# Optimization experiments

Hardware: AMD Instinct MI355X
Metric: run time of the kernel (lower is better)

## Reference

```python
import jax, jax.numpy as jnp
import numpy as np

BS, SEQ, IN, H, L = 32, 512, 1024, 1024, 2
STDV = 1.0 / np.sqrt(H)


def setup_inputs() -> dict:
    key = jax.random.key(0)
    ks = jax.random.split(key, 5)
    # params are uniform(-stdv, stdv) per reset_parameters
    u = lambda k, shape: jax.random.uniform(k, shape, jnp.float32, -STDV, STDV)
    return {
        "x": jax.random.normal(ks[0], (BS, SEQ, IN), jnp.float32),
        "w_ih": u(ks[1], (L, H, IN)),   # layer 0: [H, IN]; layer >0 uses [H, H] (IN==H here)
        "w_hh": u(ks[2], (L, H, H)),
        "b_ih": u(ks[3], (L, H)),
        "b_hh": u(ks[4], (L, H)),
    }


def _run_layer(x_sbH, w_ih_l, w_hh_l, b_ih_l, b_hh_l):
    # x_sbH: [seq, bs, in]. Precompute input projection as one GEMM.
    xproj = jnp.einsum('sbi,hi->sbh', x_sbH, w_ih_l) + b_ih_l + b_hh_l  # [seq, bs, H]

    def step(h, xp_t):
        # h_t = tanh(W_ih x_t + b_ih + W_hh h_{t-1} + b_hh)
        h_new = jnp.tanh(xp_t + h @ w_hh_l.T)
        return h_new, h_new

    h0 = jnp.zeros((x_sbH.shape[1], w_hh_l.shape[0]), x_sbH.dtype)
    h_last, hs = jax.lax.scan(step, h0, xproj)
    return hs, h_last  # hs: [seq, bs, H]


def reference(x, w_ih, w_hh, b_ih, b_hh):
    # batch_first: transpose to [seq, bs, in]
    h = jnp.transpose(x, (1, 0, 2))
    finals = []
    num_layers = w_ih.shape[0]
    for l in range(num_layers):
        h, h_last = _run_layer(h, w_ih[l], w_hh[l], b_ih[l], b_hh[l])
        finals.append(h_last)
    output = jnp.transpose(h, (1, 0, 2))           # [bs, seq, H]
    h_n = jnp.stack(finals, axis=0)                # [num_layers, bs, H]
    return output, h_n
```

## Files before the change

### kernel.cpp

```cpp
#include <hip/hip_runtime.h>

#define SEQL 512
#define BSZ  32
#define HID  1024
#define NWORK 48
#define NLAUNCH 384
#define HN_OFF 16777216

#define XPS_OFF 0u
#define H0B_OFF 33554432u
#define H1B_OFF 67108864u
#define FLG_OFF 100663296u
#define BOOT_OFF 100794368u

using f32x4  = __attribute__((ext_vector_type(4))) float;
using u16x8  = __attribute__((ext_vector_type(8))) unsigned short;
using u32x4  = __attribute__((ext_vector_type(4))) unsigned int;
using bf16x8 = __attribute__((ext_vector_type(8))) __bf16;

__device__ __forceinline__ f32x4 mfma16(u16x8 a, u16x8 b, f32x4 c) {
  return __builtin_amdgcn_mfma_f32_16x16x32_bf16(
      __builtin_bit_cast(bf16x8, a), __builtin_bit_cast(bf16x8, b), c, 0, 0, 0);
}

__device__ __forceinline__ unsigned short f2bf(float f) {
  unsigned u = __builtin_bit_cast(unsigned, f);
  u += 0x7fffu + ((u >> 16) & 1u);
  return (unsigned short)(u >> 16);
}
__device__ __forceinline__ unsigned short f2h(float f) {
  _Float16 h = (_Float16)f;
  return __builtin_bit_cast(unsigned short, h);
}
__device__ __forceinline__ float h2f(unsigned short u) {
  return (float)__builtin_bit_cast(_Float16, u);
}

__device__ __forceinline__ float tanh_fast(float x) {
  float cx = fminf(fmaxf(x, -15.f), 15.f);
  float e = __expf(2.f * cx);
  return __fdividef(e - 1.f, e + 1.f);
}

__device__ __forceinline__ void ld_tile_sc0(const unsigned short* base, u32x4 (&r)[16]) {
  const char* b0 = (const char*)base;
  const char* b1 = b0 + 16 * HID * 2;
  asm volatile(
    "global_load_dwordx4 %0, %16, off sc0\n\t"
    "global_load_dwordx4 %1, %16, off offset:64 sc0\n\t"
    "global_load_dwordx4 %2, %16, off offset:128 sc0\n\t"
    "global_load_dwordx4 %3, %16, off offset:192 sc0\n\t"
    "global_load_dwordx4 %4, %16, off offset:256 sc0\n\t"
    "global_load_dwordx4 %5, %16, off offset:320 sc0\n\t"
    "global_load_dwordx4 %6, %16, off offset:384 sc0\n\t"
    "global_load_dwordx4 %7, %16, off offset:448 sc0\n\t"
    "global_load_dwordx4 %8, %17, off sc0\n\t"
    "global_load_dwordx4 %9, %17, off offset:64 sc0\n\t"
    "global_load_dwordx4 %10, %17, off offset:128 sc0\n\t"
    "global_load_dwordx4 %11, %17, off offset:192 sc0\n\t"
    "global_load_dwordx4 %12, %17, off offset:256 sc0\n\t"
    "global_load_dwordx4 %13, %17, off offset:320 sc0\n\t"
    "global_load_dwordx4 %14, %17, off offset:384 sc0\n\t"
    "global_load_dwordx4 %15, %17, off offset:448 sc0\n\t"
    "s_waitcnt vmcnt(0)"
    : "=&v"(r[0]), "=&v"(r[1]), "=&v"(r[2]), "=&v"(r[3]),
      "=&v"(r[4]), "=&v"(r[5]), "=&v"(r[6]), "=&v"(r[7]),
      "=&v"(r[8]), "=&v"(r[9]), "=&v"(r[10]), "=&v"(r[11]),
      "=&v"(r[12]), "=&v"(r[13]), "=&v"(r[14]), "=&v"(r[15])
    : "v"(b0), "v"(b1)
    : "memory");
}

__device__ __forceinline__ u16x8 ld8h_sc0(const void* p) {
  u32x4 r;
  asm volatile("global_load_dwordx4 %0, %1, off sc0\n\ts_waitcnt vmcnt(0)"
               : "=&v"(r) : "v"(p) : "memory");
  return __builtin_bit_cast(u16x8, r);
}

__device__ __forceinline__ void flag_set(unsigned* p) {
  __hip_atomic_store(p, 1u, __ATOMIC_RELAXED, __HIP_MEMORY_SCOPE_AGENT);
}
__device__ __forceinline__ unsigned flag_get(const unsigned* p) {
  return __hip_atomic_load(p, __ATOMIC_RELAXED, __HIP_MEMORY_SCOPE_AGENT);
}

__device__ __forceinline__ void wg_wait16(const unsigned* flt, int tid) {
  if (tid < 64) {
    const unsigned* p = flt + (tid & 15);
    while (!__all(flag_get(p) != 0u)) __builtin_amdgcn_s_sleep(1);
  }
  __syncthreads();
}
__device__ __forceinline__ void wg_wait1(const unsigned* p, int tid) {
  if (tid < 64) {
    while (!__all(flag_get(p) != 0u)) __builtin_amdgcn_s_sleep(1);
  }
  __syncthreads();
}

__global__ void init_kernel(unsigned* flg, int* boot) {
  int i = blockIdx.x * 256 + threadIdx.x;
  flg[i] = 0u;
  if (blockIdx.x == 0 && threadIdx.x < 18)
    boot[threadIdx.x] = (threadIdx.x == 16) ? -1 : 0;
}

__global__ __launch_bounds__(256, 2)
void xproj_gemm(const float* __restrict__ X,
                const float* __restrict__ W,
                const float* __restrict__ bih,
                const float* __restrict__ bhh,
                unsigned short* __restrict__ out)
{
  __shared__ unsigned short sA[128 * 32];
  __shared__ unsigned short sB[128 * 32];
  const int tid  = threadIdx.x;
  const int lane = tid & 63;
  const int wave = tid >> 6;
  const int wm = wave >> 1, wn = wave & 1;
  const int bm = blockIdx.x >> 3;
  const int bn = blockIdx.x & 7;
  const int l15 = lane & 15;
  const int koff = (lane >> 4) * 8;
  const int srow = tid >> 2;
  const int skc  = (tid & 3) * 8;

  f32x4 acc[4][4];
#pragma unroll
  for (int i = 0; i < 4; ++i)
#pragma unroll
    for (int j = 0; j < 4; ++j) acc[i][j] = (f32x4)0.f;

  for (int k0 = 0; k0 < HID; k0 += 32) {
#pragma unroll
    for (int r = 0; r < 2; ++r) {
      int row = r * 64 + srow;
      int Mrow = bm * 128 + row;
      const float* src = X + ((size_t)(Mrow & 31) * SEQL + (Mrow >> 5)) * HID + k0 + skc;
      float4 a = ((const float4*)src)[0];
      float4 b = ((const float4*)src)[1];
      u16x8 av;
      av[0]=f2bf(a.x); av[1]=f2bf(a.y); av[2]=f2bf(a.z); av[3]=f2bf(a.w);
      av[4]=f2bf(b.x); av[5]=f2bf(b.y); av[6]=f2bf(b.z); av[7]=f2bf(b.w);
      *(u16x8*)&sA[row * 32 + skc] = av;

      const float* wsrc = W + (size_t)(bn * 128 + row) * HID + k0 + skc;
      float4 wa = ((const float4*)wsrc)[0];
      float4 wb = ((const float4*)wsrc)[1];
      u16x8 wv;
      wv[0]=f2bf(wa.x); wv[1]=f2bf(wa.y); wv[2]=f2bf(wa.z); wv[3]=f2bf(wa.w);
      wv[4]=f2bf(wb.x); wv[5]=f2bf(wb.y); wv[6]=f2bf(wb.z); wv[7]=f2bf(wb.w);
      *(u16x8*)&sB[row * 32 + skc] = wv;
    }
    __syncthreads();

    u16x8 af[4], bfr[4];
#pragma unroll
    for (int mt = 0; mt < 4; ++mt)
      af[mt] = *(const u16x8*)&sA[(wm * 64 + mt * 16 + l15) * 32 + koff];
#pragma unroll
    for (int nt = 0; nt < 4; ++nt)
      bfr[nt] = *(const u16x8*)&sB[(wn * 64 + nt * 16 + l15) * 32 + koff];
#pragma unroll
    for (int mt = 0; mt < 4; ++mt)
#pragma unroll
      for (int nt = 0; nt < 4; ++nt)
        acc[mt][nt] = mfma16(af[mt], bfr[nt], acc[mt][nt]);
    __syncthreads();
  }

#pragma unroll
  for (int nt = 0; nt < 4; ++nt) {
    int colg = bn * 128 + wn * 64 + nt * 16 + l15;
    float bias = bih[colg] + bhh[colg];
#pragma unroll
    for (int mt = 0; mt < 4; ++mt) {
#pragma unroll
      for (int i = 0; i < 4; ++i) {
        int rowg = bm * 128 + wm * 64 + mt * 16 + (lane >> 4) * 4 + i;
        out[(size_t)rowg * HID + colg] = f2h(acc[mt][nt][i] + bias);
      }
    }
  }
}

__global__ __launch_bounds__(256, 2)
void fused_scan(unsigned short* __restrict__ xps,
                const float* __restrict__ whh0,
                const float* __restrict__ wih1,
                const float* __restrict__ whh1,
                const float* __restrict__ bih1,
                const float* __restrict__ bhh1,
                unsigned short* __restrict__ h0b,
                unsigned short* __restrict__ h1b,
                float* __restrict__ out,
                unsigned* __restrict__ flg,
                int* __restrict__ boot)
{
  const int tid  = threadIdx.x;

  __shared__ int s_role;
  if (tid == 0) {
    unsigned xcc;
    asm volatile("s_getreg_b32 %0, hwreg(HW_REG_XCC_ID)" : "=s"(xcc));
    xcc &= 15u;
    int slot = __hip_atomic_fetch_add(&boot[(int)xcc], 1, __ATOMIC_RELAXED,
                                      __HIP_MEMORY_SCOPE_AGENT);
    if (slot == NWORK - 1) {
      int exp = -1;
      __hip_atomic_compare_exchange_strong(&boot[16], &exp, (int)xcc,
          __ATOMIC_RELAXED, __ATOMIC_RELAXED, __HIP_MEMORY_SCOPE_AGENT);
    }
    int ch;
    while ((ch = __hip_atomic_load(&boot[16], __ATOMIC_RELAXED,
                                   __HIP_MEMORY_SCOPE_AGENT)) < 0)
      __builtin_amdgcn_s_sleep(8);
    s_role = ((int)xcc == ch && slot < NWORK) ? slot : -1;
  }
  __syncthreads();
  const int role = s_role;
  if (role < 0) return;

  const int lane = tid & 63;
  const int wave = tid >> 6;
  const int l15  = lane & 15;
  const int l4   = lane >> 4;
  const int stage = role >> 4;
  const int wg    = role & 15;
  const int col0  = wg * 64;
  const int kbase = wave * 256;
  const int frow  = tid >> 3;
  const int fcb   = (tid & 7) * 8;
  const int laneoff = l15 * HID + kbase + l4 * 8;

  unsigned* flA = flg;
  unsigned* flB = flg + SEQL * 16;
  unsigned* flC = flg + 2 * SEQL * 16;

  __shared__ float red[4][32][68];

  const float* Wsl = (stage == 0) ? whh0 : (stage == 1) ? wih1 : whh1;
  u16x8 Bf[4][8];
#pragma unroll
  for (int nt = 0; nt < 4; ++nt)
#pragma unroll
    for (int ks = 0; ks < 8; ++ks) {
      const float* src = Wsl + (size_t)(col0 + nt * 16 + l15) * HID + kbase + ks * 32 + l4 * 8;
      float4 a = ((const float4*)src)[0];
      float4 b = ((const float4*)src)[1];
      u16x8 v;
      v[0]=f2bf(a.x); v[1]=f2bf(a.y); v[2]=f2bf(a.z); v[3]=f2bf(a.w);
      v[4]=f2bf(b.x); v[5]=f2bf(b.y); v[6]=f2bf(b.z); v[7]=f2bf(b.w);
      Bf[nt][ks] = v;
    }

  if (stage == 0) {
    u16x8 xh = *(const u16x8*)(xps + (size_t)frow * HID + col0 + fcb);
    for (int t = 0; t < SEQL; ++t) {
      f32x4 acc[2][4];
#pragma unroll
      for (int m = 0; m < 2; ++m)
#pragma unroll
        for (int n = 0; n < 4; ++n) acc[m][n] = (f32x4)0.f;
      if (t > 0) {
        wg_wait16(flA + (t - 1) * 16, tid);
        u32x4 r[16];
        ld_tile_sc0(h0b + (size_t)(t - 1) * (BSZ * HID) + laneoff, r);
#pragma unroll
        for (int ks = 0; ks < 8; ++ks)
#pragma unroll
          for (int m = 0; m < 2; ++m)
#pragma unroll
            for (int n = 0; n < 4; ++n)
              acc[m][n] = mfma16(__builtin_bit_cast(u16x8, r[m * 8 + ks]), Bf[n][ks], acc[m][n]);
      }
#pragma unroll
      for (int m = 0; m < 2; ++m)
#pragma unroll
        for (int n = 0; n < 4; ++n)
#pragma unroll
          for (int q = 0; q < 4; ++q)
            red[wave][m * 16 + l4 * 4 + q][n * 16 + l15] = acc[m][n][q];
      __syncthreads();
      float hv[8];
#pragma unroll
      for (int jj = 0; jj < 2; ++jj) {
        float4 r0 = *(const float4*)&red[0][frow][fcb + jj * 4];
        float4 r1 = *(const float4*)&red[1][frow][fcb + jj * 4];
        float4 r2 = *(const float4*)&red[2][frow][fcb + jj * 4];
        float4 r3 = *(const float4*)&red[3][frow][fcb + jj * 4];
        hv[jj*4+0] = r0.x + r1.x + r2.x + r3.x;
        hv[jj*4+1] = r0.y + r1.y + r2.y + r3.y;
        hv[jj*4+2] = r0.z + r1.z + r2.z + r3.z;
        hv[jj*4+3] = r0.w + r1.w + r2.w + r3.w;
      }
#pragma unroll
      for (int j = 0; j < 8; ++j) hv[j] = tanh_fast(hv[j] + h2f((unsigned short)xh[j]));
      u16x8 hb;
#pragma unroll
      for (int j = 0; j < 8; ++j) hb[j] = f2bf(hv[j]);
      *(u16x8*)(h0b + (size_t)t * (BSZ * HID) + (size_t)frow * HID + col0 + fcb) = hb;
      if (t == SEQL - 1) {
        float* o = out + HN_OFF + (size_t)frow * HID + col0 + fcb;
        ((float4*)o)[0] = make_float4(hv[0], hv[1], hv[2], hv[3]);
        ((float4*)o)[1] = make_float4(hv[4], hv[5], hv[6], hv[7]);
      } else {
        xh = *(const u16x8*)(xps + ((size_t)(t + 1) * BSZ + frow) * HID + col0 + fcb);
      }
      asm volatile("s_waitcnt vmcnt(0)" ::: "memory");
      __syncthreads();
      if (tid == 0) flag_set(&flA[t * 16 + wg]);
    }
  } else if (stage == 1) {
    float bia[8];
#pragma unroll
    for (int j = 0; j < 8; ++j)
      bia[j] = bih1[col0 + fcb + j] + bhh1[col0 + fcb + j];
    for (int t = 0; t < SEQL; ++t) {
      wg_wait16(flA + t * 16, tid);
      u32x4 r[16];
      ld_tile_sc0(h0b + (size_t)t * (BSZ * HID) + laneoff, r);
      f32x4 acc[2][4];
#pragma unroll
      for (int m = 0; m < 2; ++m)
#pragma unroll
        for (int n = 0; n < 4; ++n) acc[m][n] = (f32x4)0.f;
#pragma unroll
      for (int ks = 0; ks < 8; ++ks)
#pragma unroll
        for (int m = 0; m < 2; ++m)
#pragma unroll
          for (int n = 0; n < 4; ++n)
            acc[m][n] = mfma16(__builtin_bit_cast(u16x8, r[m * 8 + ks]), Bf[n][ks], acc[m][n]);
#pragma unroll
      for (int m = 0; m < 2; ++m)
#pragma unroll
        for (int n = 0; n < 4; ++n)
#pragma unroll
          for (int q = 0; q < 4; ++q)
            red[wave][m * 16 + l4 * 4 + q][n * 16 + l15] = acc[m][n][q];
      __syncthreads();
      float sv[8];
#pragma unroll
      for (int jj = 0; jj < 2; ++jj) {
        float4 r0 = *(const float4*)&red[0][frow][fcb + jj * 4];
        float4 r1 = *(const float4*)&red[1][frow][fcb + jj * 4];
        float4 r2 = *(const float4*)&red[2][frow][fcb + jj * 4];
        float4 r3 = *(const float4*)&red[3][frow][fcb + jj * 4];
        sv[jj*4+0] = r0.x + r1.x + r2.x + r3.x;
        sv[jj*4+1] = r0.y + r1.y + r2.y + r3.y;
        sv[jj*4+2] = r0.z + r1.z + r2.z + r3.z;
        sv[jj*4+3] = r0.w + r1.w + r2.w + r3.w;
      }
      u16x8 xo;
#pragma unroll
      for (int j = 0; j < 8; ++j) xo[j] = f2h(sv[j] + bia[j]);
      *(u16x8*)(xps + ((size_t)t * BSZ + frow) * HID + col0 + fcb) = xo;
      asm volatile("s_waitcnt vmcnt(0)" ::: "memory");
      __syncthreads();
      if (tid == 0) flag_set(&flB[t * 16 + wg]);
    }
  } else {
    for (int t = 0; t < SEQL; ++t) {
      f32x4 acc[2][4];
#pragma unroll
      for (int m = 0; m < 2; ++m)
#pragma unroll
        for (int n = 0; n < 4; ++n) acc[m][n] = (f32x4)0.f;
      if (t > 0) {
        wg_wait16(flC + (t - 1) * 16, tid);
        u32x4 r[16];
        ld_tile_sc0(h1b + (size_t)(t - 1) * (BSZ * HID) + laneoff, r);
#pragma unroll
        for (int ks = 0; ks < 8; ++ks)
#pragma unroll
          for (int m = 0; m < 2; ++m)
#pragma unroll
            for (int n = 0; n < 4; ++n)
              acc[m][n] = mfma16(__builtin_bit_cast(u16x8, r[m * 8 + ks]), Bf[n][ks], acc[m][n]);
      }
#pragma unroll
      for (int m = 0; m < 2; ++m)
#pragma unroll
        for (int n = 0; n < 4; ++n)
#pragma unroll
          for (int q = 0; q < 4; ++q)
            red[wave][m * 16 + l4 * 4 + q][n * 16 + l15] = acc[m][n][q];
      __syncthreads();
      wg_wait1(&flB[t * 16 + wg], tid);
      u16x8 xq = ld8h_sc0(xps + ((size_t)t * BSZ + frow) * HID + col0 + fcb);
      float hv[8];
#pragma unroll
      for (int jj = 0; jj < 2; ++jj) {
        float4 r0 = *(const float4*)&red[0][frow][fcb + jj * 4];
        float4 r1 = *(const float4*)&red[1][frow][fcb + jj * 4];
        float4 r2 = *(const float4*)&red[2][frow][fcb + jj * 4];
        float4 r3 = *(const float4*)&red[3][frow][fcb + jj * 4];
        hv[jj*4+0] = r0.x + r1.x + r2.x + r3.x;
        hv[jj*4+1] = r0.y + r1.y + r2.y + r3.y;
        hv[jj*4+2] = r0.z + r1.z + r2.z + r3.z;
        hv[jj*4+3] = r0.w + r1.w + r2.w + r3.w;
      }
#pragma unroll
      for (int j = 0; j < 8; ++j) hv[j] = tanh_fast(hv[j] + h2f((unsigned short)xq[j]));
      u16x8 hb;
#pragma unroll
      for (int j = 0; j < 8; ++j) hb[j] = f2bf(hv[j]);
      *(u16x8*)(h1b + (size_t)t * (BSZ * HID) + (size_t)frow * HID + col0 + fcb) = hb;
      float* op = out + ((size_t)frow * SEQL + t) * HID + col0 + fcb;
      ((float4*)op)[0] = make_float4(hv[0], hv[1], hv[2], hv[3]);
      ((float4*)op)[1] = make_float4(hv[4], hv[5], hv[6], hv[7]);
      if (t == SEQL - 1) {
        float* o = out + HN_OFF + BSZ * HID + (size_t)frow * HID + col0 + fcb;
        ((float4*)o)[0] = make_float4(hv[0], hv[1], hv[2], hv[3]);
        ((float4*)o)[1] = make_float4(hv[4], hv[5], hv[6], hv[7]);
      }
      asm volatile("s_waitcnt vmcnt(0)" ::: "memory");
      __syncthreads();
      if (tid == 0) flag_set(&flC[t * 16 + wg]);
    }
  }
}

extern "C" void kernel_launch(void* const* d_in, const int* in_sizes, int n_in,
                              void* d_out, int out_size, void* d_ws, size_t ws_size,
                              hipStream_t stream) {
  const float* x    = (const float*)d_in[0];
  const float* w_ih = (const float*)d_in[1];
  const float* w_hh = (const float*)d_in[2];
  const float* b_ih = (const float*)d_in[3];
  const float* b_hh = (const float*)d_in[4];
  float* out = (float*)d_out;
  char* ws = (char*)d_ws;

  unsigned short* xps = (unsigned short*)(ws + XPS_OFF);
  unsigned short* h0b = (unsigned short*)(ws + H0B_OFF);
  unsigned short* h1b = (unsigned short*)(ws + H1B_OFF);
  unsigned* flg       = (unsigned*)(ws + FLG_OFF);
  int* boot           = (int*)(ws + BOOT_OFF);

  init_kernel<<<96, 256, 0, stream>>>(flg, boot);
  xproj_gemm<<<1024, 256, 0, stream>>>(x, w_ih, b_ih, b_hh, xps);
  fused_scan<<<NLAUNCH, 256, 0, stream>>>(xps, w_hh,
      w_ih + (size_t)HID * HID, w_hh + (size_t)HID * HID,
      b_ih + HID, b_hh + HID, h0b, h1b, out, flg, boot);
}
```

Measured before the change: 3.589 ms.

## Spin on sc0 flag loads and use plain loads for hidden-state tiles

Flag waits now spin first with sc0 (L2-coherent, non-sleeping) loads for up to 128 iterations and only then fall back to the sleeping agent-scope atomic poll. Flag stores also issue an extra sc0 store before the atomic store. The inline-asm sc0 tile loads of the hidden state are replaced with ordinary C++ vector loads, which the compiler can schedule and interleave with the MFMAs. The aim is to cut handoff latency in the per-timestep cross-workgroup pipeline, but plain loads may hit stale data in the non-coherent L1/L2 path, which risks correctness across XCD-local workgroups.

Result: slower. 7.671 ms (+113.7%).

```diff
diff --git a/kernel.cpp b/kernel.cpp
--- a/kernel.cpp
+++ b/kernel.cpp
@@ -42,35 +42,6 @@
   return __fdividef(e - 1.f, e + 1.f);
 }
 
-__device__ __forceinline__ void ld_tile_sc0(const unsigned short* base, u32x4 (&r)[16]) {
-  const char* b0 = (const char*)base;
-  const char* b1 = b0 + 16 * HID * 2;
-  asm volatile(
-    "global_load_dwordx4 %0, %16, off sc0\n\t"
-    "global_load_dwordx4 %1, %16, off offset:64 sc0\n\t"
-    "global_load_dwordx4 %2, %16, off offset:128 sc0\n\t"
-    "global_load_dwordx4 %3, %16, off offset:192 sc0\n\t"
-    "global_load_dwordx4 %4, %16, off offset:256 sc0\n\t"
-    "global_load_dwordx4 %5, %16, off offset:320 sc0\n\t"
-    "global_load_dwordx4 %6, %16, off offset:384 sc0\n\t"
-    "global_load_dwordx4 %7, %16, off offset:448 sc0\n\t"
-    "global_load_dwordx4 %8, %17, off sc0\n\t"
-    "global_load_dwordx4 %9, %17, off offset:64 sc0\n\t"
-    "global_load_dwordx4 %10, %17, off offset:128 sc0\n\t"
-    "global_load_dwordx4 %11, %17, off offset:192 sc0\n\t"
-    "global_load_dwordx4 %12, %17, off offset:256 sc0\n\t"
-    "global_load_dwordx4 %13, %17, off offset:320 sc0\n\t"
-    "global_load_dwordx4 %14, %17, off offset:384 sc0\n\t"
-    "global_load_dwordx4 %15, %17, off offset:448 sc0\n\t"
-    "s_waitcnt vmcnt(0)"
-    : "=&v"(r[0]), "=&v"(r[1]), "=&v"(r[2]), "=&v"(r[3]),
-      "=&v"(r[4]), "=&v"(r[5]), "=&v"(r[6]), "=&v"(r[7]),
-      "=&v"(r[8]), "=&v"(r[9]), "=&v"(r[10]), "=&v"(r[11]),
-      "=&v"(r[12]), "=&v"(r[13]), "=&v"(r[14]), "=&v"(r[15])
-    : "v"(b0), "v"(b1)
-    : "memory");
-}
-
 __device__ __forceinline__ u16x8 ld8h_sc0(const void* p) {
   u32x4 r;
   asm volatile("global_load_dwordx4 %0, %1, off sc0\n\ts_waitcnt vmcnt(0)"
@@ -79,22 +50,40 @@
 }
 
 __device__ __forceinline__ void flag_set(unsigned* p) {
+  unsigned one = 1u;
+  asm volatile("global_store_dword %0, %1, off sc0" :: "v"(p), "v"(one) : "memory");
   __hip_atomic_store(p, 1u, __ATOMIC_RELAXED, __HIP_MEMORY_SCOPE_AGENT);
 }
-__device__ __forceinline__ unsigned flag_get(const unsigned* p) {
+__device__ __forceinline__ unsigned flag_get_agent(const unsigned* p) {
   return __hip_atomic_load(p, __ATOMIC_RELAXED, __HIP_MEMORY_SCOPE_AGENT);
+}
+__device__ __forceinline__ unsigned flag_get_sc0(const unsigned* p) {
+  unsigned v;
+  asm volatile("global_load_dword %0, %1, off sc0\n\ts_waitcnt vmcnt(0)"
+               : "=&v"(v) : "v"(p) : "memory");
+  return v;
 }
 
 __device__ __forceinline__ void wg_wait16(const unsigned* flt, int tid) {
   if (tid < 64) {
     const unsigned* p = flt + (tid & 15);
-    while (!__all(flag_get(p) != 0u)) __builtin_amdgcn_s_sleep(1);
+    int seen = 0;
+    for (int it = 0; it < 128 && !seen; ++it)
+      seen = __all(flag_get_sc0(p) != 0u);
+    if (!seen) {
+      while (!__all(flag_get_agent(p) != 0u)) __builtin_amdgcn_s_sleep(1);
+    }
   }
   __syncthreads();
 }
 __device__ __forceinline__ void wg_wait1(const unsigned* p, int tid) {
   if (tid < 64) {
-    while (!__all(flag_get(p) != 0u)) __builtin_amdgcn_s_sleep(1);
+    int seen = 0;
+    for (int it = 0; it < 128 && !seen; ++it)
+      seen = __all(flag_get_sc0(p) != 0u);
+    if (!seen) {
+      while (!__all(flag_get_agent(p) != 0u)) __builtin_amdgcn_s_sleep(1);
+    }
   }
   __syncthreads();
 }
@@ -232,7 +221,6 @@
   const int kbase = wave * 256;
   const int frow  = tid >> 3;
   const int fcb   = (tid & 7) * 8;
-  const int laneoff = l15 * HID + kbase + l4 * 8;
 
   unsigned* flA = flg;
   unsigned* flB = flg + SEQL * 16;
@@ -265,15 +253,20 @@
         for (int n = 0; n < 4; ++n) acc[m][n] = (f32x4)0.f;
       if (t > 0) {
         wg_wait16(flA + (t - 1) * 16, tid);
-        u32x4 r[16];
-        ld_tile_sc0(h0b + (size_t)(t - 1) * (BSZ * HID) + laneoff, r);
+        const unsigned short* hp = h0b + (size_t)(t - 1) * (BSZ * HID);
+        u16x8 Af[2][8];
+#pragma unroll
+        for (int m = 0; m < 2; ++m)
+#pragma unroll
+          for (int ks = 0; ks < 8; ++ks)
+            Af[m][ks] = *(const u16x8*)(hp + (size_t)(m * 16 + l15) * HID + kbase + ks * 32 + l4 * 8);
 #pragma unroll
         for (int ks = 0; ks < 8; ++ks)
 #pragma unroll
           for (int m = 0; m < 2; ++m)
 #pragma unroll
             for (int n = 0; n < 4; ++n)
-              acc[m][n] = mfma16(__builtin_bit_cast(u16x8, r[m * 8 + ks]), Bf[n][ks], acc[m][n]);
+              acc[m][n] = mfma16(Af[m][ks], Bf[n][ks], acc[m][n]);
       }
 #pragma unroll
       for (int m = 0; m < 2; ++m)
@@ -319,8 +312,13 @@
       bia[j] = bih1[col0 + fcb + j] + bhh1[col0 + fcb + j];
     for (int t = 0; t < SEQL; ++t) {
       wg_wait16(flA + t * 16, tid);
-      u32x4 r[16];
-      ld_tile_sc0(h0b + (size_t)t * (BSZ * HID) + laneoff, r);
+      const unsigned short* hp = h0b + (size_t)t * (BSZ * HID);
+      u16x8 Af[2][8];
+#pragma unroll
+      for (int m = 0; m < 2; ++m)
+#pragma unroll
+        for (int ks = 0; ks < 8; ++ks)
+          Af[m][ks] = *(const u16x8*)(hp + (size_t)(m * 16 + l15) * HID + kbase + ks * 32 + l4 * 8);
       f32x4 acc[2][4];
 #pragma unroll
       for (int m = 0; m < 2; ++m)
@@ -332,7 +330,7 @@
         for (int m = 0; m < 2; ++m)
 #pragma unroll
           for (int n = 0; n < 4; ++n)
-            acc[m][n] = mfma16(__builtin_bit_cast(u16x8, r[m * 8 + ks]), Bf[n][ks], acc[m][n]);
+            acc[m][n] = mfma16(Af[m][ks], Bf[n][ks], acc[m][n]);
 #pragma unroll
       for (int m = 0; m < 2; ++m)
 #pragma unroll
@@ -370,15 +368,20 @@
         for (int n = 0; n < 4; ++n) acc[m][n] = (f32x4)0.f;
       if (t > 0) {
         wg_wait16(flC + (t - 1) * 16, tid);
-        u32x4 r[16];
-        ld_tile_sc0(h1b + (size_t)(t - 1) * (BSZ * HID) + laneoff, r);
+        const unsigned short* hp = h1b + (size_t)(t - 1) * (BSZ * HID);
+        u16x8 Af[2][8];
+#pragma unroll
+        for (int m = 0; m < 2; ++m)
+#pragma unroll
+          for (int ks = 0; ks < 8; ++ks)
+            Af[m][ks] = *(const u16x8*)(hp + (size_t)(m * 16 + l15) * HID + kbase + ks * 32 + l4 * 8);
 #pragma unroll
         for (int ks = 0; ks < 8; ++ks)
 #pragma unroll
           for (int m = 0; m < 2; ++m)
 #pragma unroll
             for (int n = 0; n < 4; ++n)
-              acc[m][n] = mfma16(__builtin_bit_cast(u16x8, r[m * 8 + ks]), Bf[n][ks], acc[m][n]);
+              acc[m][n] = mfma16(Af[m][ks], Bf[n][ks], acc[m][n]);
       }
 #pragma unroll
       for (int m = 0; m < 2; ++m)
```
